# Performance work log

Hardware: AMD Instinct MI355X
Metric: run time of the kernel (lower is better)

## Reference

```python
import jax, jax.numpy as jnp
import numpy as np

N0, N1, N2, N3 = 65536, 16384, 4096, 1024
S = 9  # 3x3 kernel -> 9 selections (self + 8 directions)


def _edges(key, n):
    # each node has S incoming edges, one per selection
    src = jax.random.randint(key, (n * S,), 0, n)
    dst = jnp.repeat(jnp.arange(n), S)
    sel = jnp.tile(jnp.arange(S), n)
    return src, dst, sel


def setup_inputs() -> dict:
    key = jax.random.key(0)
    ks = jax.random.split(key, 40)
    inp = {}
    inp["x"] = jax.random.normal(ks[0], (N0, 3), jnp.float32)
    sizes = [N0, N1, N2, N3]
    for l, n in enumerate(sizes):
        src, dst, sel = _edges(ks[1 + l], n)
        inp[f"src{l}"] = src
        inp[f"dst{l}"] = dst
        inp[f"sel{l}"] = sel
        inp[f"interp{l}"] = jax.random.uniform(ks[5 + l], (n * S,), jnp.float32)
    inp["clus0"] = jnp.arange(N0) // 4
    inp["clus1"] = jnp.arange(N1) // 4
    inp["clus2"] = jnp.arange(N2) // 4
    dims = [(3, 3), (3, 64), (64, 64), (64, 128), (128, 128), (128, 256), (256, 256), (256, 256), (256, 256), (256, 512)]
    for i, (ci, co) in enumerate(dims):
        kw = ks[10 + 2 * i]
        kb = ks[11 + 2 * i]
        if i == 0:  # conv1 is kernel_size=1 -> single weight matrix
            inp["W1"] = jax.random.normal(kw, (ci, co), jnp.float32) / np.sqrt(ci).astype(np.float32)
        else:
            inp[f"W{i + 1}"] = jax.random.normal(kw, (S, ci, co), jnp.float32) / np.sqrt(S * ci).astype(np.float32)
        inp[f"b{i + 1}"] = jax.random.normal(kb, (co,), jnp.float32) * 0.01
    return inp


def _sel_conv(x, src, dst, sel, interp, W, b):
    # message = interp * x[src]; routed to (dst, selection) bucket; per-selection weight
    n = x.shape[0]
    msg = x[src] * interp[:, None]                                  # [E, Cin]
    agg = jax.ops.segment_sum(msg, dst * S + sel, num_segments=n * S)
    agg = agg.reshape(n, S, -1)                                     # [N, S, Cin]
    return jnp.einsum('nsi,sio->no', agg, W) + b


def reference(x, src0, dst0, sel0, interp0, src1, dst1, sel1, interp1,
              src2, dst2, sel2, interp2, src3, dst3, sel3, interp3,
              clus0, clus1, clus2,
              W1, b1, W2, b2, W3, b3, W4, b4, W5, b5,
              W6, b6, W7, b7, W8, b8, W9, b9, W10, b10):
    relu = jax.nn.relu
    out = x @ W1 + b1                                              # conv1 (1x1), no relu
    r11 = relu(_sel_conv(out, src0, dst0, sel0, interp0, W2, b2))
    r12 = relu(_sel_conv(r11, src0, dst0, sel0, interp0, W3, b3))
    p1 = jax.ops.segment_max(r12, clus0, num_segments=N1)
    r21 = relu(_sel_conv(p1, src1, dst1, sel1, interp1, W4, b4))
    r22 = relu(_sel_conv(r21, src1, dst1, sel1, interp1, W5, b5))
    p2 = jax.ops.segment_max(r22, clus1, num_segments=N2)
    r31 = relu(_sel_conv(p2, src2, dst2, sel2, interp2, W6, b6))
    r32 = relu(_sel_conv(r31, src2, dst2, sel2, interp2, W7, b7))
    r33 = relu(_sel_conv(r32, src2, dst2, sel2, interp2, W8, b8))
    r34 = relu(_sel_conv(r33, src2, dst2, sel2, interp2, W9, b9))
    p3 = jax.ops.segment_max(r34, clus2, num_segments=N3)
    r41 = relu(_sel_conv(p3, src3, dst3, sel3, interp3, W10, b10))
    return (r11, r12, p1, r21, r22, p2, r31, r32, r33, r34, p3, r41)
```

## Files before the change

kernel.cpp:

```cpp
#include <hip/hip_runtime.h>
#include <cstddef>


#define S9 9

typedef __attribute__((ext_vector_type(8))) _Float16 f16x8;
typedef __attribute__((ext_vector_type(4))) float f32x4;

__device__ __forceinline__ unsigned short f2h(float f) {
    _Float16 h = (_Float16)f;
    unsigned short u;
    __builtin_memcpy(&u, &h, 2);
    return u;
}

struct Pm {
    const float* x;
    const int *src0, *src1, *src2, *src3;
    const float *interp0, *interp1, *interp2, *interp3;
    const float *W1, *b1, *W2, *b2, *W3, *b3, *W4, *b4, *W5, *b5;
    const float *W6, *b6, *W7, *b7, *W8, *b8, *W9, *b9, *W10, *b10;
    float *r11, *r12, *p1, *r21, *r22, *p2, *r31, *r32, *r33, *r34, *p3, *r41;
    unsigned short *Wt3, *Wt4, *Wt5, *Wt6, *Wt7, *Wt8, *Wt9, *Wt10;
    _Float16 *a11, *ap1, *a21, *ap2, *a31, *a32, *a33, *ap3;
};

__device__ void wt_tile(const float* __restrict__ in, unsigned short* __restrict__ out,
                        int K, int N, int t, float (*sm)[33]) {
    const int ktiles = K >> 6, ntiles = N >> 5;
    const int per = ktiles * ntiles;
    const int s = t / per;
    const int rem = t - s * per;
    const int kt = rem % ktiles, nt = rem / ktiles;
    const int k0 = kt * 64, n0 = nt * 32;
    const float* ip = in + (size_t)s * K * N;
    unsigned short* op = out + (size_t)s * N * K;
    const int tx = threadIdx.x & 31;
    const int ty = threadIdx.x >> 5;
#pragma unroll
    for (int r = ty; r < 64; r += 8)
        sm[r][tx] = ip[(size_t)(k0 + r) * N + n0 + tx];
    __syncthreads();
#pragma unroll
    for (int r = ty; r < 32; r += 8) {
        unsigned v = (unsigned)f2h(sm[2 * tx][r]) |
                     ((unsigned)f2h(sm[2 * tx + 1][r]) << 16);
        *(unsigned*)&op[(size_t)(n0 + r) * K + k0 + 2 * tx] = v;
    }
}

__device__ void r11_tile(int t, const Pm& p, _Float16* As) {
    constexpr int LDA = 40;
    const int tid = threadIdx.x;
    const int wave = tid >> 6, lane = tid & 63;
    const int wr = wave >> 1, wc = wave & 1;
    const int lm = lane & 15, kq = lane >> 4;
    const int node0 = t * 64;

    const float w00 = p.W1[0], w01 = p.W1[1], w02 = p.W1[2];
    const float w10 = p.W1[3], w11 = p.W1[4], w12 = p.W1[5];
    const float w20 = p.W1[6], w21 = p.W1[7], w22 = p.W1[8];
    const float c0 = p.b1[0], c1 = p.b1[1], c2 = p.b1[2];

    for (int c = tid; c < 64 * 5; c += 256) {
        const int ln = c / 5;
        As[ln * LDA + 27 + (c - ln * 5)] = (_Float16)0.f;
    }
    for (int c = tid; c < 64 * S9; c += 256) {
        const int ln = c / S9;
        const int s = c - ln * S9;
        const int e = (node0 + ln) * S9 + s;
        const float tt = p.interp0[e];
        const float* xr = &p.x[(size_t)p.src0[e] * 3];
        const float x0 = xr[0], x1 = xr[1], x2 = xr[2];
        const float y0 = fmaf(x0, w00, fmaf(x1, w10, fmaf(x2, w20, c0)));
        const float y1 = fmaf(x0, w01, fmaf(x1, w11, fmaf(x2, w21, c1)));
        const float y2 = fmaf(x0, w02, fmaf(x1, w12, fmaf(x2, w22, c2)));
        As[ln * LDA + s * 3 + 0] = (_Float16)(tt * y0);
        As[ln * LDA + s * 3 + 1] = (_Float16)(tt * y1);
        As[ln * LDA + s * 3 + 2] = (_Float16)(tt * y2);
    }
    __syncthreads();

    f32x4 acc[2][2];
    f16x8 bfr[2];
#pragma unroll
    for (int f = 0; f < 2; ++f) {
        const int col = wc * 32 + f * 16 + lm;
#pragma unroll
        for (int j = 0; j < 8; ++j) {
            const int k = kq * 8 + j;
            bfr[f][j] = (k < 27) ? (_Float16)p.W2[k * 64 + col] : (_Float16)0.f;
        }
        const float bv = p.b2[col];
#pragma unroll
        for (int i = 0; i < 2; ++i) {
            acc[i][f][0] = bv; acc[i][f][1] = bv;
            acc[i][f][2] = bv; acc[i][f][3] = bv;
        }
    }
#pragma unroll
    for (int i = 0; i < 2; ++i) {
        const f16x8 af = *(const f16x8*)&As[(wr * 32 + i * 16 + lm) * LDA + kq * 8];
#pragma unroll
        for (int f = 0; f < 2; ++f)
            acc[i][f] = __builtin_amdgcn_mfma_f32_16x16x32_f16(af, bfr[f],
                                                               acc[i][f], 0, 0, 0);
    }
#pragma unroll
    for (int i = 0; i < 2; ++i)
#pragma unroll
        for (int f = 0; f < 2; ++f) {
            const int col = wc * 32 + f * 16 + lm;
#pragma unroll
            for (int r = 0; r < 4; ++r) {
                const int row = node0 + wr * 32 + i * 16 + kq * 4 + r;
                const float v = fmaxf(acc[i][f][r], 0.f);
                p.r11[(size_t)row * 64 + col] = v;
                p.a11[(size_t)row * 64 + col] = (_Float16)v;
            }
        }
}

__global__ __launch_bounds__(256) void prep_r11(Pm p) {
    __shared__ float sm[64][33];
    int b = blockIdx.x;
    if (b >= 1710) { r11_tile(b - 1710, p, (_Float16*)sm); return; }
    if (b < 18)              { wt_tile(p.W3,  p.Wt3,  64,  64,  b, sm); return; }
    if ((b -= 18) < 36)      { wt_tile(p.W4,  p.Wt4,  64,  128, b, sm); return; }
    if ((b -= 36) < 72)      { wt_tile(p.W5,  p.Wt5,  128, 128, b, sm); return; }
    if ((b -= 72) < 144)     { wt_tile(p.W6,  p.Wt6,  128, 256, b, sm); return; }
    if ((b -= 144) < 288)    { wt_tile(p.W7,  p.Wt7,  256, 256, b, sm); return; }
    if ((b -= 288) < 288)    { wt_tile(p.W8,  p.Wt8,  256, 256, b, sm); return; }
    if ((b -= 288) < 288)    { wt_tile(p.W9,  p.Wt9,  256, 256, b, sm); return; }
    b -= 288;                  wt_tile(p.W10, p.Wt10, 256, 512, b, sm);
}

template <int CIN, int COUT, bool POOL>
__global__ __launch_bounds__(256, 2) void selconv_wlds(
    const _Float16* __restrict__ xin, const int* __restrict__ src,
    const float* __restrict__ interp, const _Float16* __restrict__ Wt,
    const float* __restrict__ bias, float* __restrict__ out,
    _Float16* __restrict__ outh, float* __restrict__ pout,
    _Float16* __restrict__ ph) {
    static_assert(CIN % 32 == 0, "CIN multiple of 32");
    constexpr int KSTEPS = CIN / 32;
    constexpr int CPT = CIN / 32;
    constexpr int CPC = CIN / 8;
    constexpr int LDW = CIN + 8;
    __shared__ _Float16 Wlds[64 * LDW];

    const int tid = threadIdx.x;
    const int wave = tid >> 6;
    const int lane = tid & 63;
    const int wr = wave >> 1;
    const int wc = wave & 1;
    const int lm = lane & 15;
    const int kq = lane >> 4;
    const int node0 = blockIdx.x * 64;
    const int cb = blockIdx.y * 64;

    int s_lds[CPT];
    size_t s_glb[CPT];
#pragma unroll
    for (int i = 0; i < CPT; ++i) {
        const int c = tid + i * 256;
        const int col = c / CPC;
        const int off = c - col * CPC;
        s_lds[i] = col * LDW + off * 8;
        s_glb[i] = (size_t)(cb + col) * CIN + off * 8;
    }

    {
        f16x8 w[CPT];
#pragma unroll
        for (int i = 0; i < CPT; ++i) w[i] = *(const f16x8*)(Wt + s_glb[i]);
#pragma unroll
        for (int i = 0; i < CPT; ++i) *(f16x8*)&Wlds[s_lds[i]] = w[i];
    }

    f32x4 acc[2][2];
#pragma unroll
    for (int f = 0; f < 2; ++f) {
        const float bv = bias[cb + wc * 32 + f * 16 + lm];
#pragma unroll
        for (int i = 0; i < 2; ++i) {
            acc[i][f][0] = bv; acc[i][f][1] = bv;
            acc[i][f][2] = bv; acc[i][f][3] = bv;
        }
    }

    const int eb0 = (node0 + wr * 32 + lm) * S9;
    const int eb1 = eb0 + 16 * S9;
    int se0 = src[eb0], se1 = src[eb1];
    float ti0 = interp[eb0], ti1 = interp[eb1];

    __syncthreads();

#pragma unroll 1
    for (int s = 0; s < S9; ++s) {
        f16x8 av0[KSTEPS], av1[KSTEPS];
        {
            const _Float16* __restrict__ x0 = xin + (size_t)se0 * CIN + kq * 8;
            const _Float16* __restrict__ x1 = xin + (size_t)se1 * CIN + kq * 8;
#pragma unroll
            for (int kk = 0; kk < KSTEPS; ++kk) {
                av0[kk] = *(const f16x8*)(x0 + kk * 32);
                av1[kk] = *(const f16x8*)(x1 + kk * 32);
            }
        }
        const _Float16 h0 = (_Float16)ti0, h1 = (_Float16)ti1;

        if (s < S9 - 1) {
            se0 = src[eb0 + s + 1];
            se1 = src[eb1 + s + 1];
            ti0 = interp[eb0 + s + 1];
            ti1 = interp[eb1 + s + 1];
        }

        f16x8 w[CPT];
        if (s < S9 - 1) {
            const _Float16* __restrict__ Ws = Wt + (size_t)(s + 1) * COUT * CIN;
#pragma unroll
            for (int i = 0; i < CPT; ++i) w[i] = *(const f16x8*)(Ws + s_glb[i]);
        }

#pragma unroll
        for (int kk = 0; kk < KSTEPS; ++kk) {
            const f16x8 b0 =
                *(const f16x8*)&Wlds[(wc * 32 + lm) * LDW + kk * 32 + kq * 8];
            const f16x8 b1 =
                *(const f16x8*)&Wlds[(wc * 32 + 16 + lm) * LDW + kk * 32 + kq * 8];
            f16x8 a0 = av0[kk], a1 = av1[kk];
#pragma unroll
            for (int j = 0; j < 8; ++j) { a0[j] *= h0; a1[j] *= h1; }
            acc[0][0] = __builtin_amdgcn_mfma_f32_16x16x32_f16(a0, b0, acc[0][0], 0, 0, 0);
            acc[0][1] = __builtin_amdgcn_mfma_f32_16x16x32_f16(a0, b1, acc[0][1], 0, 0, 0);
            acc[1][0] = __builtin_amdgcn_mfma_f32_16x16x32_f16(a1, b0, acc[1][0], 0, 0, 0);
            acc[1][1] = __builtin_amdgcn_mfma_f32_16x16x32_f16(a1, b1, acc[1][1], 0, 0, 0);
        }

        __syncthreads();
        if (s < S9 - 1) {
#pragma unroll
            for (int i = 0; i < CPT; ++i) *(f16x8*)&Wlds[s_lds[i]] = w[i];
        }
        __syncthreads();
    }

#pragma unroll
    for (int i = 0; i < 2; ++i)
#pragma unroll
        for (int f = 0; f < 2; ++f) {
            const int col = cb + wc * 32 + f * 16 + lm;
            const int rb = node0 + wr * 32 + i * 16 + kq * 4;
            float v0 = fmaxf(acc[i][f][0], 0.f);
            float v1 = fmaxf(acc[i][f][1], 0.f);
            float v2 = fmaxf(acc[i][f][2], 0.f);
            float v3 = fmaxf(acc[i][f][3], 0.f);
            out[(size_t)(rb + 0) * COUT + col] = v0;
            out[(size_t)(rb + 1) * COUT + col] = v1;
            out[(size_t)(rb + 2) * COUT + col] = v2;
            out[(size_t)(rb + 3) * COUT + col] = v3;
            if (outh) {
                outh[(size_t)(rb + 0) * COUT + col] = (_Float16)v0;
                outh[(size_t)(rb + 1) * COUT + col] = (_Float16)v1;
                outh[(size_t)(rb + 2) * COUT + col] = (_Float16)v2;
                outh[(size_t)(rb + 3) * COUT + col] = (_Float16)v3;
            }
            if constexpr (POOL) {
                const float m = fmaxf(fmaxf(v0, v1), fmaxf(v2, v3));
                const int prow = rb >> 2;
                pout[(size_t)prow * COUT + col] = m;
                ph[(size_t)prow * COUT + col] = (_Float16)m;
            }
        }
}

extern "C" void kernel_launch(void* const* d_in, const int* in_sizes, int n_in,
                              void* d_out, int out_size, void* d_ws, size_t ws_size,
                              hipStream_t stream) {
    Pm p;
    p.x = (const float*)d_in[0];
    p.src0 = (const int*)d_in[1];
    p.interp0 = (const float*)d_in[4];
    p.src1 = (const int*)d_in[5];
    p.interp1 = (const float*)d_in[8];
    p.src2 = (const int*)d_in[9];
    p.interp2 = (const float*)d_in[12];
    p.src3 = (const int*)d_in[13];
    p.interp3 = (const float*)d_in[16];
    p.W1 = (const float*)d_in[20];  p.b1 = (const float*)d_in[21];
    p.W2 = (const float*)d_in[22];  p.b2 = (const float*)d_in[23];
    p.W3 = (const float*)d_in[24];  p.b3 = (const float*)d_in[25];
    p.W4 = (const float*)d_in[26];  p.b4 = (const float*)d_in[27];
    p.W5 = (const float*)d_in[28];  p.b5 = (const float*)d_in[29];
    p.W6 = (const float*)d_in[30];  p.b6 = (const float*)d_in[31];
    p.W7 = (const float*)d_in[32];  p.b7 = (const float*)d_in[33];
    p.W8 = (const float*)d_in[34];  p.b8 = (const float*)d_in[35];
    p.W9 = (const float*)d_in[36];  p.b9 = (const float*)d_in[37];
    p.W10 = (const float*)d_in[38]; p.b10 = (const float*)d_in[39];

    float* out = (float*)d_out;
    p.r11 = out;
    p.r12 = p.r11 + (size_t)65536 * 64;
    p.p1  = p.r12 + (size_t)65536 * 64;
    p.r21 = p.p1 + (size_t)16384 * 64;
    p.r22 = p.r21 + (size_t)16384 * 128;
    p.p2  = p.r22 + (size_t)16384 * 128;
    p.r31 = p.p2 + (size_t)4096 * 128;
    p.r32 = p.r31 + (size_t)4096 * 256;
    p.r33 = p.r32 + (size_t)4096 * 256;
    p.r34 = p.r33 + (size_t)4096 * 256;
    p.p3  = p.r34 + (size_t)4096 * 256;
    p.r41 = p.p3 + (size_t)1024 * 256;

    unsigned short* w16 = (unsigned short*)d_ws;
    p.Wt3 = w16;
    p.Wt4 = p.Wt3 + (size_t)9 * 64 * 64;
    p.Wt5 = p.Wt4 + (size_t)9 * 128 * 64;
    p.Wt6 = p.Wt5 + (size_t)9 * 128 * 128;
    p.Wt7 = p.Wt6 + (size_t)9 * 256 * 128;
    p.Wt8 = p.Wt7 + (size_t)9 * 256 * 256;
    p.Wt9 = p.Wt8 + (size_t)9 * 256 * 256;
    p.Wt10 = p.Wt9 + (size_t)9 * 256 * 256;
    unsigned short* endw = p.Wt10 + (size_t)9 * 512 * 256;
    p.a11 = (_Float16*)endw;
    p.ap1 = p.a11 + (size_t)65536 * 64;
    p.a21 = p.ap1 + (size_t)16384 * 64;
    p.ap2 = p.a21 + (size_t)16384 * 128;
    p.a31 = p.ap2 + (size_t)4096 * 128;
    p.a32 = p.a31 + (size_t)4096 * 256;
    p.a33 = p.a32 + (size_t)4096 * 256;
    p.ap3 = p.a33 + (size_t)4096 * 256;

    prep_r11<<<2734, 256, 0, stream>>>(p);

    selconv_wlds<64, 64, true><<<dim3(1024, 1), 256, 0, stream>>>(
        p.a11, p.src0, p.interp0, (const _Float16*)p.Wt3, p.b3, p.r12,
        nullptr, p.p1, p.ap1);

    selconv_wlds<64, 128, false><<<dim3(256, 2), 256, 0, stream>>>(
        p.ap1, p.src1, p.interp1, (const _Float16*)p.Wt4, p.b4, p.r21,
        p.a21, nullptr, nullptr);

    selconv_wlds<128, 128, true><<<dim3(256, 2), 256, 0, stream>>>(
        p.a21, p.src1, p.interp1, (const _Float16*)p.Wt5, p.b5, p.r22,
        nullptr, p.p2, p.ap2);

    selconv_wlds<128, 256, false><<<dim3(64, 4), 256, 0, stream>>>(
        p.ap2, p.src2, p.interp2, (const _Float16*)p.Wt6, p.b6, p.r31,
        p.a31, nullptr, nullptr);

    selconv_wlds<256, 256, false><<<dim3(64, 4), 256, 0, stream>>>(
        p.a31, p.src2, p.interp2, (const _Float16*)p.Wt7, p.b7, p.r32,
        p.a32, nullptr, nullptr);
    selconv_wlds<256, 256, false><<<dim3(64, 4), 256, 0, stream>>>(
        p.a32, p.src2, p.interp2, (const _Float16*)p.Wt8, p.b8, p.r33,
        p.a33, nullptr, nullptr);
    selconv_wlds<256, 256, true><<<dim3(64, 4), 256, 0, stream>>>(
        p.a33, p.src2, p.interp2, (const _Float16*)p.Wt9, p.b9, p.r34,
        nullptr, p.p3, p.ap3);

    selconv_wlds<256, 512, false><<<dim3(16, 8), 256, 0, stream>>>(
        p.ap3, p.src3, p.interp3, (const _Float16*)p.Wt10, p.b10, p.r41,
        nullptr, nullptr, nullptr);
}
```

Before: 370.5 us.

## Double-buffer weight slabs via direct global-to-LDS loads with XOR swizzle

The selection-conv kernel now stages each per-selection weight slab straight into LDS with global_load_lds and keeps two slabs in flight, replacing the register round-trip and the two block barriers per step with one barrier per step under explicit vmcnt waits. The gathers of neighbour features and src/interp indices are software-pipelined one selection ahead, and the weight transpose writes an XOR-swizzled layout so LDS reads avoid bank conflicts without padding. This hides weight and gather latency behind MFMA work, at the cost of doubled LDS use (which may lower occupancy for CIN=256) and fragile hand-counted vmcnt waits and scheduling barriers.

```diff
diff --git a/kernel.cpp b/kernel.cpp
--- a/kernel.cpp
+++ b/kernel.cpp
@@ -13,6 +13,21 @@
     __builtin_memcpy(&u, &h, 2);
     return u;
 }
+
+__device__ __forceinline__ void gload_lds16(const void* g, void* l) {
+    __builtin_amdgcn_global_load_lds(
+        (const __attribute__((address_space(1))) void*)g,
+        (__attribute__((address_space(3))) void*)l, 16, 0, 0);
+}
+
+__device__ __forceinline__ void sb0() { __builtin_amdgcn_sched_barrier(0); }
+
+template <int N> __device__ __forceinline__ void wait_vm();
+template <> __device__ __forceinline__ void wait_vm<4>()  { asm volatile("s_waitcnt vmcnt(4)" ::: "memory"); }
+template <> __device__ __forceinline__ void wait_vm<8>()  { asm volatile("s_waitcnt vmcnt(8)" ::: "memory"); }
+template <> __device__ __forceinline__ void wait_vm<12>() { asm volatile("s_waitcnt vmcnt(12)" ::: "memory"); }
+template <> __device__ __forceinline__ void wait_vm<16>() { asm volatile("s_waitcnt vmcnt(16)" ::: "memory"); }
+template <> __device__ __forceinline__ void wait_vm<20>() { asm volatile("s_waitcnt vmcnt(20)" ::: "memory"); }
 
 struct Pm {
     const float* x;
@@ -34,7 +49,7 @@
     const int kt = rem % ktiles, nt = rem / ktiles;
     const int k0 = kt * 64, n0 = nt * 32;
     const float* ip = in + (size_t)s * K * N;
-    unsigned short* op = out + (size_t)s * N * K;
+    char* op = (char*)(out + (size_t)s * N * K);
     const int tx = threadIdx.x & 31;
     const int ty = threadIdx.x >> 5;
 #pragma unroll
@@ -45,7 +60,10 @@
     for (int r = ty; r < 32; r += 8) {
         unsigned v = (unsigned)f2h(sm[2 * tx][r]) |
                      ((unsigned)f2h(sm[2 * tx + 1][r]) << 16);
-        *(unsigned*)&op[(size_t)(n0 + r) * K + k0 + 2 * tx] = v;
+        const int gcol = n0 + r;
+        const int ob = 2 * (k0 + 2 * tx);
+        const int obs = (ob & ~15) ^ ((gcol & 7) << 4);
+        *(unsigned*)(op + (size_t)gcol * (K * 2) + obs + (ob & 15)) = v;
     }
 }
 
@@ -137,18 +155,17 @@
 }
 
 template <int CIN, int COUT, bool POOL>
-__global__ __launch_bounds__(256, 2) void selconv_wlds(
+__global__ __launch_bounds__(256, 2) void selconv_cnt(
     const _Float16* __restrict__ xin, const int* __restrict__ src,
     const float* __restrict__ interp, const _Float16* __restrict__ Wt,
     const float* __restrict__ bias, float* __restrict__ out,
     _Float16* __restrict__ outh, float* __restrict__ pout,
     _Float16* __restrict__ ph) {
     static_assert(CIN % 32 == 0, "CIN multiple of 32");
-    constexpr int KSTEPS = CIN / 32;
-    constexpr int CPT = CIN / 32;
-    constexpr int CPC = CIN / 8;
-    constexpr int LDW = CIN + 8;
-    __shared__ _Float16 Wlds[64 * LDW];
+    constexpr int K = CIN / 32;
+    constexpr int SLABH = 64 * CIN;
+    constexpr int SLABB = SLABH * 2;
+    __shared__ _Float16 Wlds[2 * SLABH];
 
     const int tid = threadIdx.x;
     const int wave = tid >> 6;
@@ -160,24 +177,19 @@
     const int node0 = blockIdx.x * 64;
     const int cb = blockIdx.y * 64;
 
-    int s_lds[CPT];
-    size_t s_glb[CPT];
-#pragma unroll
-    for (int i = 0; i < CPT; ++i) {
-        const int c = tid + i * 256;
-        const int col = c / CPC;
-        const int off = c - col * CPC;
-        s_lds[i] = col * LDW + off * 8;
-        s_glb[i] = (size_t)(cb + col) * CIN + off * 8;
-    }
-
-    {
-        f16x8 w[CPT];
-#pragma unroll
-        for (int i = 0; i < CPT; ++i) w[i] = *(const f16x8*)(Wt + s_glb[i]);
-#pragma unroll
-        for (int i = 0; i < CPT; ++i) *(f16x8*)&Wlds[s_lds[i]] = w[i];
-    }
+    const int colA = wc * 32 + lm;
+    const int colB = colA + 16;
+    const int xg = (lm & 7) << 4;
+    const int baseA = colA * CIN * 2;
+    const int baseB = colB * CIN * 2;
+
+    const _Float16* __restrict__ Wcb = Wt + (size_t)cb * CIN + tid * 8;
+    auto stage = [&](int s, int bufOff) {
+#pragma unroll
+        for (int i = 0; i < K; ++i)
+            gload_lds16(Wcb + (size_t)s * COUT * CIN + i * 2048,
+                        (char*)Wlds + bufOff + (i * 256 + wave * 64) * 16);
+    };
 
     f32x4 acc[2][2];
 #pragma unroll
@@ -192,46 +204,29 @@
 
     const int eb0 = (node0 + wr * 32 + lm) * S9;
     const int eb1 = eb0 + 16 * S9;
-    int se0 = src[eb0], se1 = src[eb1];
-    float ti0 = interp[eb0], ti1 = interp[eb1];
-
-    __syncthreads();
-
-#pragma unroll 1
-    for (int s = 0; s < S9; ++s) {
-        f16x8 av0[KSTEPS], av1[KSTEPS];
-        {
-            const _Float16* __restrict__ x0 = xin + (size_t)se0 * CIN + kq * 8;
-            const _Float16* __restrict__ x1 = xin + (size_t)se1 * CIN + kq * 8;
-#pragma unroll
-            for (int kk = 0; kk < KSTEPS; ++kk) {
-                av0[kk] = *(const f16x8*)(x0 + kk * 32);
-                av1[kk] = *(const f16x8*)(x1 + kk * 32);
-            }
-        }
-        const _Float16 h0 = (_Float16)ti0, h1 = (_Float16)ti1;
-
-        if (s < S9 - 1) {
-            se0 = src[eb0 + s + 1];
-            se1 = src[eb1 + s + 1];
-            ti0 = interp[eb0 + s + 1];
-            ti1 = interp[eb1 + s + 1];
-        }
-
-        f16x8 w[CPT];
-        if (s < S9 - 1) {
-            const _Float16* __restrict__ Ws = Wt + (size_t)(s + 1) * COUT * CIN;
-#pragma unroll
-            for (int i = 0; i < CPT; ++i) w[i] = *(const f16x8*)(Ws + s_glb[i]);
-        }
-
-#pragma unroll
-        for (int kk = 0; kk < KSTEPS; ++kk) {
-            const f16x8 b0 =
-                *(const f16x8*)&Wlds[(wc * 32 + lm) * LDW + kk * 32 + kq * 8];
-            const f16x8 b1 =
-                *(const f16x8*)&Wlds[(wc * 32 + 16 + lm) * LDW + kk * 32 + kq * 8];
-            f16x8 a0 = av0[kk], a1 = av1[kk];
+
+    f16x8 avA0[K], avA1[K], avB0[K], avB1[K];
+    _Float16 hA0, hA1, hB0, hB1;
+    int seA0, seA1, seB0, seB1;
+    float tiA0, tiA1, tiB0, tiB1;
+
+    auto gather = [&](int se0, int se1, f16x8* v0, f16x8* v1) {
+        const _Float16* __restrict__ x0 = xin + (size_t)se0 * CIN + kq * 8;
+        const _Float16* __restrict__ x1 = xin + (size_t)se1 * CIN + kq * 8;
+#pragma unroll
+        for (int kk = 0; kk < K; ++kk) {
+            v0[kk] = *(const f16x8*)(x0 + kk * 32);
+            v1[kk] = *(const f16x8*)(x1 + kk * 32);
+        }
+    };
+    auto compute = [&](const f16x8* v0, const f16x8* v1, _Float16 h0,
+                       _Float16 h1, int slabOff) {
+#pragma unroll
+        for (int kk = 0; kk < K; ++kk) {
+            const int off = (kk * 64 + kq * 16) ^ xg;
+            const f16x8 b0 = *(const f16x8*)((const char*)Wlds + slabOff + baseA + off);
+            const f16x8 b1 = *(const f16x8*)((const char*)Wlds + slabOff + baseB + off);
+            f16x8 a0 = v0[kk], a1 = v1[kk];
 #pragma unroll
             for (int j = 0; j < 8; ++j) { a0[j] *= h0; a1[j] *= h1; }
             acc[0][0] = __builtin_amdgcn_mfma_f32_16x16x32_f16(a0, b0, acc[0][0], 0, 0, 0);
@@ -239,14 +234,85 @@
             acc[1][0] = __builtin_amdgcn_mfma_f32_16x16x32_f16(a1, b0, acc[1][0], 0, 0, 0);
             acc[1][1] = __builtin_amdgcn_mfma_f32_16x16x32_f16(a1, b1, acc[1][1], 0, 0, 0);
         }
-
-        __syncthreads();
-        if (s < S9 - 1) {
-#pragma unroll
-            for (int i = 0; i < CPT; ++i) *(f16x8*)&Wlds[s_lds[i]] = w[i];
-        }
-        __syncthreads();
-    }
+    };
+
+    seA0 = src[eb0]; seA1 = src[eb1];
+    tiA0 = interp[eb0]; tiA1 = interp[eb1];
+    sb0();
+    stage(0, 0);
+    sb0();
+    seB0 = src[eb0 + 1]; seB1 = src[eb1 + 1];
+    tiB0 = interp[eb0 + 1]; tiB1 = interp[eb1 + 1];
+    sb0();
+    gather(seA0, seA1, avA0, avA1);
+    hA0 = (_Float16)tiA0; hA1 = (_Float16)tiA1;
+    sb0();
+    wait_vm<2 * K + 4>();
+    sb0();
+    __builtin_amdgcn_s_barrier();
+    sb0();
+
+#pragma unroll 1
+    for (int t = 0; t < 3; ++t) {
+        const int s0 = 2 * t;
+        stage(s0 + 1, SLABB);
+        sb0();
+        seA0 = src[eb0 + s0 + 2]; seA1 = src[eb1 + s0 + 2];
+        tiA0 = interp[eb0 + s0 + 2]; tiA1 = interp[eb1 + s0 + 2];
+        sb0();
+        gather(seB0, seB1, avB0, avB1);
+        hB0 = (_Float16)tiB0; hB1 = (_Float16)tiB1;
+        sb0();
+        compute(avA0, avA1, hA0, hA1, 0);
+        sb0();
+        wait_vm<2 * K + 4>();
+        sb0();
+        __builtin_amdgcn_s_barrier();
+        sb0();
+        stage(s0 + 2, 0);
+        sb0();
+        seB0 = src[eb0 + s0 + 3]; seB1 = src[eb1 + s0 + 3];
+        tiB0 = interp[eb0 + s0 + 3]; tiB1 = interp[eb1 + s0 + 3];
+        sb0();
+        gather(seA0, seA1, avA0, avA1);
+        hA0 = (_Float16)tiA0; hA1 = (_Float16)tiA1;
+        sb0();
+        compute(avB0, avB1, hB0, hB1, SLABB);
+        sb0();
+        wait_vm<2 * K + 4>();
+        sb0();
+        __builtin_amdgcn_s_barrier();
+        sb0();
+    }
+
+    stage(7, SLABB);
+    sb0();
+    seA0 = src[eb0 + 8]; seA1 = src[eb1 + 8];
+    tiA0 = interp[eb0 + 8]; tiA1 = interp[eb1 + 8];
+    sb0();
+    gather(seB0, seB1, avB0, avB1);
+    hB0 = (_Float16)tiB0; hB1 = (_Float16)tiB1;
+    sb0();
+    compute(avA0, avA1, hA0, hA1, 0);
+    sb0();
+    wait_vm<2 * K + 4>();
+    sb0();
+    __builtin_amdgcn_s_barrier();
+    sb0();
+
+    stage(8, 0);
+    sb0();
+    gather(seA0, seA1, avA0, avA1);
+    hA0 = (_Float16)tiA0; hA1 = (_Float16)tiA1;
+    sb0();
+    compute(avB0, avB1, hB0, hB1, SLABB);
+    sb0();
+    wait_vm<2 * K>();
+    sb0();
+    __builtin_amdgcn_s_barrier();
+    sb0();
+
+    compute(avA0, avA1, hA0, hA1, 0);
 
 #pragma unroll
     for (int i = 0; i < 2; ++i)
@@ -336,33 +402,33 @@
 
     prep_r11<<<2734, 256, 0, stream>>>(p);
 
-    selconv_wlds<64, 64, true><<<dim3(1024, 1), 256, 0, stream>>>(
+    selconv_cnt<64, 64, true><<<dim3(1024, 1), 256, 0, stream>>>(
         p.a11, p.src0, p.interp0, (const _Float16*)p.Wt3, p.b3, p.r12,
         nullptr, p.p1, p.ap1);
 
-    selconv_wlds<64, 128, false><<<dim3(256, 2), 256, 0, stream>>>(
+    selconv_cnt<64, 128, false><<<dim3(256, 2), 256, 0, stream>>>(
         p.ap1, p.src1, p.interp1, (const _Float16*)p.Wt4, p.b4, p.r21,
         p.a21, nullptr, nullptr);
 
-    selconv_wlds<128, 128, true><<<dim3(256, 2), 256, 0, stream>>>(
+    selconv_cnt<128, 128, true><<<dim3(256, 2), 256, 0, stream>>>(
         p.a21, p.src1, p.interp1, (const _Float16*)p.Wt5, p.b5, p.r22,
         nullptr, p.p2, p.ap2);
 
-    selconv_wlds<128, 256, false><<<dim3(64, 4), 256, 0, stream>>>(
+    selconv_cnt<128, 256, false><<<dim3(64, 4), 256, 0, stream>>>(
         p.ap2, p.src2, p.interp2, (const _Float16*)p.Wt6, p.b6, p.r31,
         p.a31, nullptr, nullptr);
 
-    selconv_wlds<256, 256, false><<<dim3(64, 4), 256, 0, stream>>>(
+    selconv_cnt<256, 256, false><<<dim3(64, 4), 256, 0, stream>>>(
         p.a31, p.src2, p.interp2, (const _Float16*)p.Wt7, p.b7, p.r32,
         p.a32, nullptr, nullptr);
-    selconv_wlds<256, 256, false><<<dim3(64, 4), 256, 0, stream>>>(
+    selconv_cnt<256, 256, false><<<dim3(64, 4), 256, 0, stream>>>(
         p.a32, p.src2, p.interp2, (const _Float16*)p.Wt8, p.b8, p.r33,
         p.a33, nullptr, nullptr);
-    selconv_wlds<256, 256, true><<<dim3(64, 4), 256, 0, stream>>>(
+    selconv_cnt<256, 256, true><<<dim3(64, 4), 256, 0, stream>>>(
         p.a33, p.src2, p.interp2, (const _Float16*)p.Wt9, p.b9, p.r34,
         nullptr, p.p3, p.ap3);
 
-    selconv_wlds<256, 512, false><<<dim3(16, 8), 256, 0, stream>>>(
+    selconv_cnt<256, 512, false><<<dim3(16, 8), 256, 0, stream>>>(
         p.ap3, p.src3, p.interp3, (const _Float16*)p.Wt10, p.b10, p.r41,
         nullptr, nullptr, nullptr);
 }
```

Result: faster. 362.7 us (-2.1%).
